# Kernel tuning notes

Hardware: AMD Instinct MI355X
Metric: run time of the kernel (lower is better)

Reference implementation:

```python
import jax, jax.numpy as jnp
import numpy as np

B, S, D, E, TOPK, H = 8, 2048, 2048, 8, 2, 16
DH = D // H          # head_dim = 128
FH = D // H          # head_hidden_dim = 128 (hidden == dim, forced by linear3 shapes)
ROUTE_LEN = 2048     # x0 = x[:, :2048]


def setup_inputs() -> dict:
    key = jax.random.key(0)
    ks = jax.random.split(key, 8)
    s = 0.02
    return {
        "x": jax.random.normal(ks[0], (B, S, D), jnp.float32),
        "switch_w": jax.random.normal(ks[1], (E, D * ROUTE_LEN), jnp.float32) * s,
        "switch_b": jnp.zeros((E,), jnp.float32),
        "w1": jax.random.normal(ks[2], (E, FH, DH), jnp.float32) * s,
        "b1": jnp.zeros((E, FH), jnp.float32),
        "w2": jax.random.normal(ks[3], (E, DH, FH), jnp.float32) * s,
        "b2": jnp.zeros((E, DH), jnp.float32),
        "w3": jax.random.normal(ks[4], (D, D), jnp.float32) * s,
        "b3": jnp.zeros((D,), jnp.float32),
    }


def reference(x, switch_w, switch_b, w1, b1, w2, b2, w3, b3):
    b, s, d = x.shape
    # --- router: per batch-sample softmax over experts, top-k selection ---
    x0 = x[:, :ROUTE_LEN].reshape(b, -1)                      # [B, 2048*D]
    logits = x0 @ switch_w.T + switch_b                       # [B, E]
    probs = jax.nn.softmax(logits, axis=-1)
    gate, top_idx = jax.lax.top_k(probs, TOPK)                # [B, K]
    # --- split heads ---
    xh = x.reshape(b, s, H, DH).transpose(0, 2, 1, 3)         # [B, H, S, Dh]
    # --- per-sample gather of selected expert weights (dense grouped GEMM) ---
    w1s, b1s = w1[top_idx], b1[top_idx]                       # [B,K,F,Dh], [B,K,F]
    w2s, b2s = w2[top_idx], b2[top_idx]                       # [B,K,Dh,F], [B,K,Dh]
    h = jnp.einsum('bhsd,bkfd->bkhsf', xh, w1s) + b1s[:, :, None, None, :]
    h = jax.nn.gelu(h, approximate=False)                     # torch nn.GELU is exact
    o = jnp.einsum('bkhsf,bkdf->bkhsd', h, w2s) + b2s[:, :, None, None, :]
    # gate-weighted combine over selected experts (index_add_ sums the k copies)
    o = (o * gate[:, :, None, None, None]).sum(axis=1)        # [B, H, S, Dh]
    o = o.transpose(0, 2, 1, 3).reshape(b, s, d)              # combine heads
    out = x + o                                               # residual
    return out @ w3.T + b3                                    # linear3
```

## Files before the change

kernel.cpp:

```cpp
#include <hip/hip_runtime.h>
#include <math.h>

typedef unsigned short u16;
typedef unsigned int u32;
typedef __attribute__((ext_vector_type(8))) short short8;
typedef __attribute__((ext_vector_type(4))) float f32x4;
typedef __attribute__((ext_vector_type(4))) unsigned short ushort4v;

#define B_ 8
#define S_ 2048
#define D_ 2048
#define H_ 16
#define RLEN 4194304
#define NCHUNK 512

static __device__ __forceinline__ u16 f2bf(float f) {
    union { float f; u32 u; } v; v.f = f;
    u32 r = v.u + 0x7fffu + ((v.u >> 16) & 1u);
    return (u16)(r >> 16);
}
static __device__ __forceinline__ float bf2f(u16 u) {
    union { u32 u; float f; } v; v.u = ((u32)u) << 16;
    return v.f;
}
static __device__ __forceinline__ float gelu_fast(float v) {
    float z = 1.5957691216057308f * v * (1.0f + 0.044715f * v * v);
    float e = __expf(z);
    float r = __builtin_amdgcn_rcpf(e + 1.0f);
    return v * (1.0f - r);
}

typedef const __attribute__((address_space(1))) u32* gas1_t;
typedef __attribute__((address_space(3))) u32* las3_t;
static __device__ __forceinline__ void gload_lds16(const void* g, void* l) {
    __builtin_amdgcn_global_load_lds((gas1_t)g, (las3_t)l, 16, 0, 0);
}

template<int XB>
__global__ __launch_bounds__(256) void router_partial(const float* __restrict__ x,
                                                      const float* __restrict__ sw,
                                                      float* __restrict__ part,
                                                      u16* __restrict__ xb) {
    int c = blockIdx.x;
    int t = threadIdx.x;
    const int chunk = RLEN / NCHUNK;
    int base = c * chunk;
    float acc[8][8];
#pragma unroll
    for (int b = 0; b < 8; b++)
#pragma unroll
        for (int e = 0; e < 8; e++) acc[b][e] = 0.f;

    for (int it = 0; it < chunk / (256 * 4); ++it) {
        int i = base + (it * 256 + t) * 4;
        float4 xv[8], sv[8];
#pragma unroll
        for (int b = 0; b < 8; b++) xv[b] = *(const float4*)&x[(size_t)b * RLEN + i];
#pragma unroll
        for (int e = 0; e < 8; e++) sv[e] = *(const float4*)&sw[(size_t)e * RLEN + i];
        if (XB) {
            int row = i >> 7, col = i & 127;
            int scol = (((col >> 3) ^ (row & 7)) << 3) | (col & 7);
#pragma unroll
            for (int b = 0; b < 8; b++) {
                ushort4v u;
                u.x = f2bf(xv[b].x); u.y = f2bf(xv[b].y);
                u.z = f2bf(xv[b].z); u.w = f2bf(xv[b].w);
                *(ushort4v*)&xb[(size_t)b * RLEN + (size_t)row * 128 + scol] = u;
            }
        }
#pragma unroll
        for (int b = 0; b < 8; b++)
#pragma unroll
            for (int e = 0; e < 8; e++)
                acc[b][e] += xv[b].x * sv[e].x + xv[b].y * sv[e].y +
                             xv[b].z * sv[e].z + xv[b].w * sv[e].w;
    }

    __shared__ float red[4][64];
    int lane = t & 63, wv = t >> 6;
#pragma unroll
    for (int q = 0; q < 64; q++) {
        float v = acc[q >> 3][q & 7];
#pragma unroll
        for (int m = 32; m >= 1; m >>= 1) v += __shfl_xor(v, m, 64);
        if (lane == 0) red[wv][q] = v;
    }
    __syncthreads();
    if (t < 64) {
        float s = red[0][t] + red[1][t] + red[2][t] + red[3][t];
        part[(size_t)t * NCHUNK + c] = s;
    }
}

__global__ __launch_bounds__(128) void router_finish(const float* __restrict__ part,
                                                     const float* __restrict__ swb,
                                                     const float* __restrict__ b2,
                                                     float* __restrict__ gate,
                                                     int* __restrict__ idx,
                                                     float* __restrict__ bc) {
    int t = threadIdx.x;
    __shared__ float lg[64];
    __shared__ float sg[16];
    __shared__ int   si[16];
    if (t < 64) {
        float s = 0.f;
        for (int c = 0; c < NCHUNK; c++) s += part[(size_t)t * NCHUNK + c];
        lg[t] = s + swb[t & 7];
    }
    __syncthreads();
    if (t < 8) {
        int b = t;
        float m = -1e30f;
        for (int e = 0; e < 8; e++) m = fmaxf(m, lg[b * 8 + e]);
        float p[8]; float sum = 0.f;
        for (int e = 0; e < 8; e++) { p[e] = expf(lg[b * 8 + e] - m); sum += p[e]; }
        for (int e = 0; e < 8; e++) p[e] /= sum;
        int i1 = 0; float v1 = p[0];
        for (int e = 1; e < 8; e++) if (p[e] > v1) { v1 = p[e]; i1 = e; }
        int i2 = -1; float v2 = -1.f;
        for (int e = 0; e < 8; e++) if (e != i1 && p[e] > v2) { v2 = p[e]; i2 = e; }
        gate[b * 2 + 0] = v1; gate[b * 2 + 1] = v2;
        idx[b * 2 + 0] = i1;  idx[b * 2 + 1] = i2;
        sg[b * 2] = v1; sg[b * 2 + 1] = v2;
        si[b * 2] = i1; si[b * 2 + 1] = i2;
    }
    __syncthreads();
    for (int b = 0; b < 8; b++)
        bc[b * 128 + t] = sg[b * 2] * b2[si[b * 2] * 128 + t] +
                          sg[b * 2 + 1] * b2[si[b * 2 + 1] * 128 + t];
}

__global__ __launch_bounds__(256) void convert_w12(const float* __restrict__ w1,
                                                   const float* __restrict__ w2,
                                                   u16* __restrict__ w1b,
                                                   u16* __restrict__ w2b) {
    int i4 = (blockIdx.x * 256 + threadIdx.x) * 4;
    if (i4 < 131072) {
        int k = i4 & 127, f = (i4 >> 7) & 127;
        float4 v = *(const float4*)&w1[i4];
        int sc = ((((k >> 3) ^ (f & 7)) << 3) | (k & 7));
        ushort4v u;
        u.x = f2bf(v.x); u.y = f2bf(v.y); u.z = f2bf(v.z); u.w = f2bf(v.w);
        *(ushort4v*)&w1b[(i4 & ~127) + sc] = u;
    } else {
        int j = i4 - 131072;
        float4 v = *(const float4*)&w2[j];
        ushort4v u;
        u.x = f2bf(v.x); u.y = f2bf(v.y); u.z = f2bf(v.z); u.w = f2bf(v.w);
        *(ushort4v*)&w2b[j] = u;
    }
}

__global__ __launch_bounds__(256) void convert_w3(const float* __restrict__ w3,
                                                  u16* __restrict__ w3b) {
    size_t i = ((size_t)blockIdx.x * 256 + threadIdx.x) * 4;
    float4 v = *(const float4*)&w3[i];
    u16* d = &w3b[i];
    d[0] = f2bf(v.x); d[1] = f2bf(v.y); d[2] = f2bf(v.z); d[3] = f2bf(v.w);
}

template<int XB>
__global__ __launch_bounds__(512) void mlp_kernel(const void* __restrict__ xsrc_,
                                                  const u16* __restrict__ w1b,
                                                  const u16* __restrict__ w2b,
                                                  const float* __restrict__ b1,
                                                  const float* __restrict__ gate,
                                                  const int* __restrict__ idx,
                                                  const float* __restrict__ bc,
                                                  u16* __restrict__ y) {
    __shared__ __align__(16) u16 w1s[256 * 128];
    __shared__ __align__(16) u16 xs[2][64 * 128];
    __shared__ __align__(16) u16 hb[2][32 * 256];
    const int t = threadIdx.x, lane = t & 63, w = t >> 6;
    const int wr = w >> 2, wq = w & 3;
    const int l15 = lane & 15, l4 = lane >> 4;
    const int b = blockIdx.y, grp = blockIdx.x;
    const size_t xbase = (size_t)b * RLEN;
    const size_t gbase = xbase + (size_t)grp * 65536;
    const int e0 = idx[b * 2], e1 = idx[b * 2 + 1];
    const int slot = wq >> 1;
    const float gw = gate[b * 2 + slot];
    const float* b1p = b1 + (slot ? e1 : e0) * 128;

    float b1v[4];
#pragma unroll
    for (int nt = 0; nt < 4; nt++) b1v[nt] = b1p[(wq & 1) * 64 + nt * 16 + l15];
    float bcv[2];
#pragma unroll
    for (int n = 0; n < 2; n++) bcv[n] = bc[b * 128 + wq * 32 + n * 16 + l15];

    short8 w2f[2][8];
#pragma unroll
    for (int n = 0; n < 2; n++) {
        int d = wq * 32 + n * 16 + l15;
#pragma unroll
        for (int kb = 0; kb < 8; kb++) {
            int e = (kb >= 4) ? e1 : e0;
            int f = (kb & 3) * 32 + l4 * 8;
            w2f[n][kb] = *(const short8*)&w2b[((size_t)(e * 128 + d)) * 128 + f];
        }
    }

#pragma unroll
    for (int p = 0; p < 8; p++) {
        int elem = p * 4096 + t * 8;
        int frow = elem >> 7, col = elem & 127;
        int e = (frow >= 128) ? e1 : e0;
        gload_lds16(w1b + ((size_t)(e * 128 + (frow & 127))) * 128 + col,
                    (char*)w1s + elem * 2);
    }
    if (XB) {
        const u16* xbp = (const u16*)xsrc_;
#pragma unroll
        for (int T = 0; T < 2; T++)
            gload_lds16(xbp + gbase + T * 8192 + t * 8, (char*)&xs[T][0] + t * 16);
#pragma unroll
        for (int T = 0; T < 2; T++)
            gload_lds16(xbp + gbase + T * 8192 + 4096 + t * 8,
                        (char*)&xs[T][0] + 8192 + t * 16);
        asm volatile("s_waitcnt vmcnt(0)" ::: "memory");
    } else {
        const float* xf = (const float*)xsrc_;
#pragma unroll
        for (int T = 0; T < 2; T++)
#pragma unroll
            for (int p = 0; p < 4; p++) {
                int elem = p * 2048 + t * 4;
                int row = elem >> 7, col = elem & 127;
                float4 v = *(const float4*)&xf[gbase + T * 8192 + elem];
                ushort4v u;
                u.x = f2bf(v.x); u.y = f2bf(v.y); u.z = f2bf(v.z); u.w = f2bf(v.w);
                *(ushort4v*)((char*)&xs[T][0] + row * 256 +
                             (((col >> 3) ^ (row & 7)) << 4) + (col & 7) * 2) = u;
            }
        asm volatile("s_waitcnt vmcnt(0) lgkmcnt(0)" ::: "memory");
    }
    __builtin_amdgcn_s_barrier();

    auto G1 = [&](int st, f32x4* a1) {
        const u16* xc = &xs[(st >> 1) & 1][0];
        int rbase = (st & 1) * 32 + wr * 16 + l15;
#pragma unroll
        for (int nt = 0; nt < 4; nt++) a1[nt] = (f32x4){0.f, 0.f, 0.f, 0.f};
#pragma unroll
        for (int kb = 0; kb < 4; kb++) {
            int kg = kb * 4 + l4;
            short8 a = *(const short8*)&xc[rbase * 128 + ((kg ^ (rbase & 7)) << 3)];
#pragma unroll
            for (int nt = 0; nt < 4; nt++) {
                int fr = wq * 64 + nt * 16 + l15;
                short8 bb = *(const short8*)&w1s[fr * 128 + ((kg ^ (fr & 7)) << 3)];
                a1[nt] = __builtin_amdgcn_mfma_f32_16x16x32_bf16(a, bb, a1[nt], 0, 0, 0);
            }
        }
    };
    auto GELU_ST = [&](int st, f32x4* a1) {
        u16* hd = &hb[st & 1][0];
#pragma unroll
        for (int nt = 0; nt < 4; nt++) {
            int fcol = wq * 64 + nt * 16 + l15;
#pragma unroll
            for (int j = 0; j < 4; j++) {
                int row = wr * 16 + l4 * 4 + j;
                float v = a1[nt][j] + b1v[nt];
                v = gelu_fast(v) * gw;
                hd[row * 256 + ((((fcol >> 3) ^ (row & 7)) << 3) | (fcol & 7))] = f2bf(v);
            }
        }
    };
    auto G2 = [&](int st, f32x4* a2) {
        const u16* hs = &hb[st & 1][0];
        int arow = wr * 16 + l15;
        a2[0] = (f32x4){0.f, 0.f, 0.f, 0.f};
        a2[1] = (f32x4){0.f, 0.f, 0.f, 0.f};
#pragma unroll
        for (int kb = 0; kb < 8; kb++) {
            int fg = kb * 4 + l4;
            short8 a = *(const short8*)&hs[arow * 256 + ((fg ^ (arow & 7)) << 3)];
            a2[0] = __builtin_amdgcn_mfma_f32_16x16x32_bf16(a, w2f[0][kb], a2[0], 0, 0, 0);
            a2[1] = __builtin_amdgcn_mfma_f32_16x16x32_bf16(a, w2f[1][kb], a2[1], 0, 0, 0);
        }
    };
    auto YST = [&](int st, f32x4* a2) {
        const u16* xc = &xs[(st >> 1) & 1][0];
        u16* yb = y + xbase + (size_t)grp * 65536 + st * 4096;
#pragma unroll
        for (int n = 0; n < 2; n++) {
            int d = wq * 32 + n * 16 + l15;
#pragma unroll
            for (int j = 0; j < 4; j++) {
                int row = wr * 16 + l4 * 4 + j;
                int xrow = (st & 1) * 32 + row;
                float xr = bf2f(xc[xrow * 128 + ((((d >> 3) ^ (xrow & 7)) << 3) | (d & 7))]);
                yb[row * 128 + d] = f2bf(a2[n][j] + bcv[n] + xr);
            }
        }
    };

    {
        f32x4 a1[4];
        G1(0, a1);
        GELU_ST(0, a1);
    }
    asm volatile("s_waitcnt lgkmcnt(0)" ::: "memory");
    __builtin_amdgcn_s_barrier();

    for (int st = 0; st < 16; ++st) {
        const bool stg = ((st & 1) == 0) && st >= 2 && st <= 12;
        if (stg) {
            int T = st / 2 + 1;
            if (XB) {
                const u16* xbp = (const u16*)xsrc_;
                gload_lds16(xbp + gbase + T * 8192 + t * 8, (char*)&xs[T & 1][0] + t * 16);
                gload_lds16(xbp + gbase + T * 8192 + 4096 + t * 8,
                            (char*)&xs[T & 1][0] + 8192 + t * 16);
            } else {
                const float* xf = (const float*)xsrc_;
#pragma unroll
                for (int p = 0; p < 4; p++) {
                    int elem = p * 2048 + t * 4;
                    int row = elem >> 7, col = elem & 127;
                    float4 v = *(const float4*)&xf[gbase + T * 8192 + elem];
                    ushort4v u;
                    u.x = f2bf(v.x); u.y = f2bf(v.y); u.z = f2bf(v.z); u.w = f2bf(v.w);
                    *(ushort4v*)((char*)&xs[T & 1][0] + row * 256 +
                                 (((col >> 3) ^ (row & 7)) << 4) + (col & 7) * 2) = u;
                }
            }
        }
        f32x4 a1n[4];
        if (st < 15) G1(st + 1, a1n);
        f32x4 a2[2];
        G2(st, a2);
        if (st < 15) GELU_ST(st + 1, a1n);
        YST(st, a2);
        asm volatile("s_waitcnt lgkmcnt(0)" ::: "memory");
        if (stg && XB) asm volatile("s_waitcnt vmcnt(8)" ::: "memory");
        if (stg && !XB) asm volatile("s_waitcnt vmcnt(0)" ::: "memory");
        __builtin_amdgcn_s_barrier();
    }
}

#define BARX() do { asm volatile("" ::: "memory"); __builtin_amdgcn_s_barrier(); \
                    asm volatile("" ::: "memory"); } while (0)
#define WLGC(NSTR) do { asm volatile("s_waitcnt lgkmcnt(" NSTR ")" ::: "memory"); \
                        __builtin_amdgcn_sched_barrier(0); } while (0)
#define WVMC(NSTR) do { asm volatile("s_waitcnt vmcnt(" NSTR ")" ::: "memory"); \
                        __builtin_amdgcn_sched_barrier(0); } while (0)

#define DSA(mh, c) do { \
    const char* _ba = smem + (c) * 65536 + abase; \
    _Pragma("unroll") for (int mf = 0; mf < 4; mf++) \
    _Pragma("unroll") for (int kk = 0; kk < 2; kk++) \
        areg[mf][kk] = *(const short8*)(_ba + ((mh) * 4 + mf) * 2048 + kof[kk]); \
} while (0)

#define DSB(nh, c) do { \
    const char* _bb = smem + (c) * 65536 + bbase; \
    _Pragma("unroll") for (int nf = 0; nf < 2; nf++) \
    _Pragma("unroll") for (int kk = 0; kk < 2; kk++) \
        breg[(nh) * 2 + nf][kk] = *(const short8*)(_bb + ((nh) * 2 + nf) * 2048 + kof[kk]); \
} while (0)

#define MMAQ(mh, nh) do { \
    __builtin_amdgcn_s_setprio(1); \
    _Pragma("unroll") for (int mf = 0; mf < 4; mf++) \
    _Pragma("unroll") for (int nf = 0; nf < 2; nf++) \
    _Pragma("unroll") for (int kk = 0; kk < 2; kk++) \
        acc[(mh) * 4 + mf][(nh) * 2 + nf] = __builtin_amdgcn_mfma_f32_16x16x32_bf16( \
            areg[mf][kk], breg[(nh) * 2 + nf][kk], acc[(mh) * 4 + mf][(nh) * 2 + nf], 0, 0, 0); \
    __builtin_amdgcn_s_setprio(0); \
} while (0)

#define STG(op, c, h, kt) do { \
    const u16* _gs = (op) ? wbp : yap; \
    int _tr0 = (op) ? nrow0 : mrow0; \
    _Pragma("unroll") for (int p = 0; p < 2; p++) { \
        int _idx = p * 512 + t; \
        int _row = _idx >> 3; \
        int _gcol = (((_idx & 7) ^ (_row & 7)) << 3); \
        gload_lds16(_gs + (size_t)(_tr0 + (h) * 128 + _row) * 2048 + (kt) * 64 + _gcol, \
                    smem + (c) * 65536 + (op) * 32768 + (h) * 16384 + _idx * 16); \
    } \
} while (0)

__global__ __launch_bounds__(512, 2) void final_gemm256(const u16* __restrict__ yap,
                                                        const u16* __restrict__ wbp,
                                                        const float* __restrict__ b3,
                                                        float* __restrict__ out) {
    extern __shared__ char smem[];
    const int t = threadIdx.x;
    const int lane = t & 63, w = t >> 6;
    const int wm = w >> 2, wn = w & 3;
    const int l15 = lane & 15, l4 = lane >> 4, sx = lane & 7;

    int bid = blockIdx.x;
    int swz = (bid & 7) * 64 + (bid >> 3);
    int nblk = swz >> 6, mblk = swz & 63;
    const int mrow0 = mblk * 256;
    const int nrow0 = nblk * 256;

    const int abase = wm * 16384 + l15 * 128;
    const int bbase = 32768 + (wn >> 1) * 16384 + ((wn & 1) * 64 + l15) * 128;
    int kof[2];
#pragma unroll
    for (int kk = 0; kk < 2; kk++) kof[kk] = ((kk * 4 + l4) ^ sx) << 4;

    f32x4 acc[8][4];
#pragma unroll
    for (int m = 0; m < 8; m++)
#pragma unroll
        for (int n = 0; n < 4; n++) acc[m][n] = (f32x4){0.f, 0.f, 0.f, 0.f};
    short8 areg[4][2];
    short8 breg[4][2];

    STG(0, 0, 0, 0); STG(0, 0, 1, 0); STG(1, 0, 0, 0); STG(1, 0, 1, 0);
    STG(0, 1, 0, 1); STG(1, 1, 0, 1); STG(1, 1, 1, 1); STG(0, 1, 1, 1);
    WVMC("8");
    BARX();

    for (int tt = 0; tt < 30; ++tt) {
        const int c = tt & 1;
        DSA(0, c); DSB(0, c);
        if (tt >= 1) STG(1, c ^ 1, 1, tt + 1);
        WLGC("8");
        BARX(); WLGC("0"); MMAQ(0, 0);
        WVMC("8"); BARX();
        DSB(1, c);
        if (tt >= 1) STG(0, c ^ 1, 1, tt + 1);
        BARX(); WLGC("0"); MMAQ(0, 1);
        WVMC("8"); BARX();
        DSA(1, c);
        STG(0, c, 0, tt + 2);
        BARX(); WLGC("0"); MMAQ(1, 0);
        WVMC("8"); BARX();
        STG(1, c, 0, tt + 2);
        BARX(); MMAQ(1, 1);
        WVMC("8"); BARX();
    }
    {
        const int c = 0;
        DSA(0, c); DSB(0, c); STG(1, c ^ 1, 1, 31);
        WLGC("8"); BARX(); WLGC("0"); MMAQ(0, 0);
        WVMC("8"); BARX();
        DSB(1, c); STG(0, c ^ 1, 1, 31);
        BARX(); WLGC("0"); MMAQ(0, 1);
        WVMC("8"); BARX();
        DSA(1, c);
        BARX(); WLGC("0"); MMAQ(1, 0);
        WVMC("4"); BARX();
        BARX(); MMAQ(1, 1);
        WVMC("4"); BARX();
    }
    {
        const int c = 1;
        DSA(0, c); DSB(0, c);
        WLGC("8"); BARX(); WLGC("0"); MMAQ(0, 0);
        WVMC("2"); BARX();
        DSB(1, c);
        BARX(); WLGC("0"); MMAQ(0, 1);
        WVMC("0"); BARX();
        DSA(1, c);
        BARX(); WLGC("0"); MMAQ(1, 0);
        BARX();
        MMAQ(1, 1);
    }

#pragma unroll
    for (int m = 0; m < 8; m++)
#pragma unroll
        for (int n = 0; n < 4; n++) {
            int col = nrow0 + wn * 64 + n * 16 + l15;
            float bias = b3[col];
            int row = mrow0 + wm * 128 + m * 16 + l4 * 4;
#pragma unroll
            for (int j = 0; j < 4; j++)
                out[(size_t)(row + j) * 2048 + col] = acc[m][n][j] + bias;
        }
}

extern "C" void kernel_launch(void* const* d_in, const int* in_sizes, int n_in,
                              void* d_out, int out_size, void* d_ws, size_t ws_size,
                              hipStream_t stream) {
    const float* x   = (const float*)d_in[0];
    const float* sw  = (const float*)d_in[1];
    const float* swb = (const float*)d_in[2];
    const float* w1  = (const float*)d_in[3];
    const float* b1  = (const float*)d_in[4];
    const float* w2  = (const float*)d_in[5];
    const float* b2  = (const float*)d_in[6];
    const float* w3  = (const float*)d_in[7];
    const float* b3  = (const float*)d_in[8];
    float* out = (float*)d_out;

    char* ws = (char*)d_ws;
    float* part = (float*)(ws + 0);
    float* gate = (float*)(ws + 131072);
    int*   idx  = (int*)(ws + 131136);
    float* bc   = (float*)(ws + 131200);
    u16*   w1b  = (u16*)(ws + 262144);
    u16*   w2b  = (u16*)(ws + 524288);
    u16*   w3b  = (u16*)(ws + 786432);
    u16*   y    = (u16*)(ws + 9175040);
    u16*   xb   = (u16*)(ws + 76283904);
    const size_t need_xb = 143392768;
    const bool xbmode = ws_size >= need_xb;

    hipFuncSetAttribute((const void*)final_gemm256,
                        hipFuncAttributeMaxDynamicSharedMemorySize, 131072);

    if (xbmode)
        hipLaunchKernelGGL((router_partial<1>), dim3(NCHUNK), dim3(256), 0, stream, x, sw, part, xb);
    else
        hipLaunchKernelGGL((router_partial<0>), dim3(NCHUNK), dim3(256), 0, stream, x, sw, part, xb);
    hipLaunchKernelGGL(router_finish, dim3(1), dim3(128), 0, stream, part, swb, b2, gate, idx, bc);
    hipLaunchKernelGGL(convert_w12, dim3(256), dim3(256), 0, stream, w1, w2, w1b, w2b);
    hipLaunchKernelGGL(convert_w3, dim3(D_ * D_ / 1024), dim3(256), 0, stream, w3, w3b);
    if (xbmode)
        hipLaunchKernelGGL((mlp_kernel<1>), dim3(64, 8), dim3(512), 0, stream,
                           (const void*)xb, w1b, w2b, b1, gate, idx, bc, y);
    else
        hipLaunchKernelGGL((mlp_kernel<0>), dim3(64, 8), dim3(512), 0, stream,
                           (const void*)x, w1b, w2b, b1, gate, idx, bc, y);
    hipLaunchKernelGGL(final_gemm256, dim3(512), dim3(512), 131072, stream,
                       y, w3b, b3, out);
}
```

Before: 334.8 us.

## Rework router loads, stage MLP output via LDS, simplify GEMM pipeline

```diff
diff --git a/kernel.cpp b/kernel.cpp
--- a/kernel.cpp
+++ b/kernel.cpp
@@ -37,10 +37,10 @@
 }
 
 template<int XB>
-__global__ __launch_bounds__(256) void router_partial(const float* __restrict__ x,
-                                                      const float* __restrict__ sw,
-                                                      float* __restrict__ part,
-                                                      u16* __restrict__ xb) {
+__global__ __launch_bounds__(256, 3) void router_partial(const float* __restrict__ x,
+                                                         const float* __restrict__ sw,
+                                                         float* __restrict__ part,
+                                                         u16* __restrict__ xb) {
     int c = blockIdx.x;
     int t = threadIdx.x;
     const int chunk = RLEN / NCHUNK;
@@ -53,11 +53,9 @@
 
     for (int it = 0; it < chunk / (256 * 4); ++it) {
         int i = base + (it * 256 + t) * 4;
-        float4 xv[8], sv[8];
+        float4 xv[8];
 #pragma unroll
         for (int b = 0; b < 8; b++) xv[b] = *(const float4*)&x[(size_t)b * RLEN + i];
-#pragma unroll
-        for (int e = 0; e < 8; e++) sv[e] = *(const float4*)&sw[(size_t)e * RLEN + i];
         if (XB) {
             int row = i >> 7, col = i & 127;
             int scol = (((col >> 3) ^ (row & 7)) << 3) | (col & 7);
@@ -69,12 +67,17 @@
                 *(ushort4v*)&xb[(size_t)b * RLEN + (size_t)row * 128 + scol] = u;
             }
         }
-#pragma unroll
-        for (int b = 0; b < 8; b++)
-#pragma unroll
-            for (int e = 0; e < 8; e++)
-                acc[b][e] += xv[b].x * sv[e].x + xv[b].y * sv[e].y +
-                             xv[b].z * sv[e].z + xv[b].w * sv[e].w;
+        float4 sv = *(const float4*)&sw[i];
+#pragma unroll
+        for (int e = 0; e < 8; e++) {
+            float4 svn;
+            if (e < 7) svn = *(const float4*)&sw[(size_t)(e + 1) * RLEN + i];
+#pragma unroll
+            for (int b = 0; b < 8; b++)
+                acc[b][e] += xv[b].x * sv.x + xv[b].y * sv.y +
+                             xv[b].z * sv.z + xv[b].w * sv.w;
+            sv = svn;
+        }
     }
 
     __shared__ float red[4][64];
@@ -172,6 +175,7 @@
     __shared__ __align__(16) u16 w1s[256 * 128];
     __shared__ __align__(16) u16 xs[2][64 * 128];
     __shared__ __align__(16) u16 hb[2][32 * 256];
+    __shared__ __align__(16) u16 ob[2][32 * 128];
     const int t = threadIdx.x, lane = t & 63, w = t >> 6;
     const int wr = w >> 2, wq = w & 3;
     const int l15 = lane & 15, l4 = lane >> 4;
@@ -213,12 +217,11 @@
     if (XB) {
         const u16* xbp = (const u16*)xsrc_;
 #pragma unroll
-        for (int T = 0; T < 2; T++)
+        for (int T = 0; T < 2; T++) {
             gload_lds16(xbp + gbase + T * 8192 + t * 8, (char*)&xs[T][0] + t * 16);
-#pragma unroll
-        for (int T = 0; T < 2; T++)
             gload_lds16(xbp + gbase + T * 8192 + 4096 + t * 8,
                         (char*)&xs[T][0] + 8192 + t * 16);
+        }
         asm volatile("s_waitcnt vmcnt(0)" ::: "memory");
     } else {
         const float* xf = (const float*)xsrc_;
@@ -282,9 +285,9 @@
             a2[1] = __builtin_amdgcn_mfma_f32_16x16x32_bf16(a, w2f[1][kb], a2[1], 0, 0, 0);
         }
     };
-    auto YST = [&](int st, f32x4* a2) {
+    auto OWRITE = [&](int st, f32x4* a2) {
+        u16* od = &ob[st & 1][0];
         const u16* xc = &xs[(st >> 1) & 1][0];
-        u16* yb = y + xbase + (size_t)grp * 65536 + st * 4096;
 #pragma unroll
         for (int n = 0; n < 2; n++) {
             int d = wq * 32 + n * 16 + l15;
@@ -293,9 +296,17 @@
                 int row = wr * 16 + l4 * 4 + j;
                 int xrow = (st & 1) * 32 + row;
                 float xr = bf2f(xc[xrow * 128 + ((((d >> 3) ^ (xrow & 7)) << 3) | (d & 7))]);
-                yb[row * 128 + d] = f2bf(a2[n][j] + bcv[n] + xr);
+                od[row * 128 + (d ^ ((row & 7) << 3))] = f2bf(a2[n][j] + bcv[n] + xr);
             }
         }
+    };
+    auto YSTV = [&](int st) {
+        int row = t >> 4;
+        int cg = t & 15;
+        const u16* os = &ob[st & 1][0];
+        short8 v = *(const short8*)&os[row * 128 + ((cg ^ (row & 7)) << 3)];
+        u16* yb = y + xbase + (size_t)grp * 65536 + st * 4096;
+        *(short8*)&yb[row * 128 + cg * 8] = v;
     };
 
     {
@@ -306,8 +317,16 @@
     asm volatile("s_waitcnt lgkmcnt(0)" ::: "memory");
     __builtin_amdgcn_s_barrier();
 
-    for (int st = 0; st < 16; ++st) {
-        const bool stg = ((st & 1) == 0) && st >= 2 && st <= 12;
+    for (int st = 0; st < 17; ++st) {
+        const bool stg = (st < 16) && ((st & 1) == 0) && st >= 2 && st <= 12;
+        if (st < 16) {
+            f32x4 a1n[4];
+            if (st < 15) G1(st + 1, a1n);
+            f32x4 a2[2];
+            G2(st, a2);
+            if (st < 15) GELU_ST(st + 1, a1n);
+            OWRITE(st, a2);
+        }
         if (stg) {
             int T = st / 2 + 1;
             if (XB) {
@@ -329,25 +348,18 @@
                 }
             }
         }
-        f32x4 a1n[4];
-        if (st < 15) G1(st + 1, a1n);
-        f32x4 a2[2];
-        G2(st, a2);
-        if (st < 15) GELU_ST(st + 1, a1n);
-        YST(st, a2);
+        if (st >= 1) YSTV(st - 1);
         asm volatile("s_waitcnt lgkmcnt(0)" ::: "memory");
-        if (stg && XB) asm volatile("s_waitcnt vmcnt(8)" ::: "memory");
-        if (stg && !XB) asm volatile("s_waitcnt vmcnt(0)" ::: "memory");
-        __builtin_amdgcn_s_barrier();
+        if (stg && XB) asm volatile("s_waitcnt vmcnt(1)" ::: "memory");
+        if (st < 16) __builtin_amdgcn_s_barrier();
     }
 }
 
 #define BARX() do { asm volatile("" ::: "memory"); __builtin_amdgcn_s_barrier(); \
                     asm volatile("" ::: "memory"); } while (0)
-#define WLGC(NSTR) do { asm volatile("s_waitcnt lgkmcnt(" NSTR ")" ::: "memory"); \
-                        __builtin_amdgcn_sched_barrier(0); } while (0)
-#define WVMC(NSTR) do { asm volatile("s_waitcnt vmcnt(" NSTR ")" ::: "memory"); \
-                        __builtin_amdgcn_sched_barrier(0); } while (0)
+
+#define WLG(NSTR) do { asm volatile("s_waitcnt lgkmcnt(" NSTR ")" ::: "memory"); \
+                       __builtin_amdgcn_sched_barrier(0); } while (0)
 
 #define DSA(mh, c) do { \
     const char* _ba = smem + (c) * 65536 + abase; \
@@ -416,55 +428,26 @@
     short8 breg[4][2];
 
     STG(0, 0, 0, 0); STG(0, 0, 1, 0); STG(1, 0, 0, 0); STG(1, 0, 1, 0);
-    STG(0, 1, 0, 1); STG(1, 1, 0, 1); STG(1, 1, 1, 1); STG(0, 1, 1, 1);
-    WVMC("8");
+    STG(0, 1, 0, 1); STG(0, 1, 1, 1); STG(1, 1, 0, 1); STG(1, 1, 1, 1);
+    asm volatile("s_waitcnt vmcnt(8)" ::: "memory");
     BARX();
-
-    for (int tt = 0; tt < 30; ++tt) {
-        const int c = tt & 1;
-        DSA(0, c); DSB(0, c);
-        if (tt >= 1) STG(1, c ^ 1, 1, tt + 1);
-        WLGC("8");
-        BARX(); WLGC("0"); MMAQ(0, 0);
-        WVMC("8"); BARX();
-        DSB(1, c);
-        if (tt >= 1) STG(0, c ^ 1, 1, tt + 1);
-        BARX(); WLGC("0"); MMAQ(0, 1);
-        WVMC("8"); BARX();
-        DSA(1, c);
-        STG(0, c, 0, tt + 2);
-        BARX(); WLGC("0"); MMAQ(1, 0);
-        WVMC("8"); BARX();
-        STG(1, c, 0, tt + 2);
-        BARX(); MMAQ(1, 1);
-        WVMC("8"); BARX();
-    }
-    {
-        const int c = 0;
-        DSA(0, c); DSB(0, c); STG(1, c ^ 1, 1, 31);
-        WLGC("8"); BARX(); WLGC("0"); MMAQ(0, 0);
-        WVMC("8"); BARX();
-        DSB(1, c); STG(0, c ^ 1, 1, 31);
-        BARX(); WLGC("0"); MMAQ(0, 1);
-        WVMC("8"); BARX();
-        DSA(1, c);
-        BARX(); WLGC("0"); MMAQ(1, 0);
-        WVMC("4"); BARX();
-        BARX(); MMAQ(1, 1);
-        WVMC("4"); BARX();
-    }
-    {
-        const int c = 1;
-        DSA(0, c); DSB(0, c);
-        WLGC("8"); BARX(); WLGC("0"); MMAQ(0, 0);
-        WVMC("2"); BARX();
-        DSB(1, c);
-        BARX(); WLGC("0"); MMAQ(0, 1);
-        WVMC("0"); BARX();
-        DSA(1, c);
-        BARX(); WLGC("0"); MMAQ(1, 0);
-        BARX();
-        MMAQ(1, 1);
+    DSA(0, 0); DSB(0, 0); DSB(1, 0);
+
+    for (int it2 = 0; it2 < 16; ++it2) {
+#pragma unroll
+        for (int c = 0; c < 2; ++c) {
+            const int tt = 2 * it2 + c;
+            WLG("4");  MMAQ(0, 0);
+            WLG("0");  MMAQ(0, 1);
+            DSA(1, c);
+            WLG("0");  MMAQ(1, 0);
+            asm volatile("s_waitcnt vmcnt(0)" ::: "memory");
+            BARX();
+            if (tt < 30) { STG(0, c, 0, tt + 2); STG(0, c, 1, tt + 2);
+                           STG(1, c, 0, tt + 2); STG(1, c, 1, tt + 2); }
+            MMAQ(1, 1);
+            if (tt < 31) { DSA(0, c ^ 1); DSB(0, c ^ 1); DSB(1, c ^ 1); }
+        }
     }
 
 #pragma unroll
```

Result: faster. 325.5 us (-2.8%).
